# Kernel optimization log

Measured on AMD Instinct MI355X. Metric: run time of the kernel, lower is better.

Reference implementation:

```python
import jax, jax.numpy as jnp
import numpy as np

INPUT_DIM = 512
HIDDEN_DIM = 256
REP_DIM = 256
SCORE_HIDDEN = 128


def setup_inputs() -> dict:
    key = jax.random.key(0)
    ks = jax.random.split(key, 12)
    def rn(k, shape, scale=None):
        s = scale if scale is not None else 1.0 / np.sqrt(shape[0])
        return jax.random.normal(k, shape, dtype=jnp.float32) * s
    return {
        "feat_x": jax.random.normal(ks[0], (512, INPUT_DIM), dtype=jnp.float32),
        "feat_pos": jax.random.normal(ks[1], (512, INPUT_DIM), dtype=jnp.float32),
        "feat_neg": jax.random.normal(ks[2], (512, INPUT_DIM), dtype=jnp.float32),
        # g: Linear(input,hidden) -> GELU -> Linear(hidden,rep); stored as x @ W
        "g_w1": rn(ks[3], (INPUT_DIM, HIDDEN_DIM)),
        "g_b1": jnp.zeros((HIDDEN_DIM,), jnp.float32),
        "g_w2": rn(ks[4], (HIDDEN_DIM, REP_DIM)),
        "g_b2": jnp.zeros((REP_DIM,), jnp.float32),
        # out_proj: Linear(rep, input, bias=False)
        "out_w": rn(ks[5], (REP_DIM, INPUT_DIM)),
        # score_net: Linear(3*rep+1, score_hidden) -> GELU -> Linear(score_hidden, 1)
        "s_w1": rn(ks[6], (3 * REP_DIM + 1, SCORE_HIDDEN)),
        "s_b1": jnp.zeros((SCORE_HIDDEN,), jnp.float32),
        "s_w2": rn(ks[7], (SCORE_HIDDEN, 1)),
        "s_b2": jnp.zeros((1,), jnp.float32),
    }


def _gelu(x):
    return jax.nn.gelu(x, approximate=False)  # torch nn.GELU default = exact erf


def _g(x, g_w1, g_b1, g_w2, g_b2):
    return _gelu(x @ g_w1 + g_b1) @ g_w2 + g_b2


def _set_operator(feat_x, feat_set, params):
    g_w1, g_b1, g_w2, g_b2, out_w, s_w1, s_b1, s_w2, s_b2 = params
    x_rep = _g(feat_x, g_w1, g_b1, g_w2, g_b2)   # (n, r)
    y_rep = _g(feat_set, g_w1, g_b1, g_w2, g_b2)  # (m, r)
    n, r = x_rep.shape
    m = y_rep.shape[0]
    x_exp = jnp.broadcast_to(x_rep[:, None, :], (n, m, r))
    y_exp = jnp.broadcast_to(y_rep[None, :, :], (n, m, r))
    delta = y_exp - x_exp                                   # (n, m, r)
    delta_norm = jnp.linalg.norm(delta, axis=-1, keepdims=True)
    score_in = jnp.concatenate([x_exp, y_exp, delta, delta_norm], axis=-1)  # (n, m, 3r+1)
    logits = (_gelu(score_in @ s_w1 + s_b1) @ s_w2 + s_b2)[..., 0]          # (n, m)
    weights = jax.nn.softmax(logits, axis=1)
    set_update_rep = jnp.einsum("nm,nmr->nr", weights, delta)
    return set_update_rep @ out_w


def reference(feat_x, feat_pos, feat_neg, g_w1, g_b1, g_w2, g_b2, out_w, s_w1, s_b1, s_w2, s_b2):
    params = (g_w1, g_b1, g_w2, g_b2, out_w, s_w1, s_b1, s_w2, s_b2)
    s_pos = _set_operator(feat_x, feat_pos, params)
    s_neg = _set_operator(feat_x, feat_neg, params)  # mask_self_neg=False
    return s_pos - s_neg
```

## Files before the change

### kernel.cpp

```cpp
#include <hip/hip_runtime.h>
#include <math.h>

#define NN 512
#define IN 512
#define HD 256
#define RD 256
#define SH 128

__device__ __forceinline__ float gelu_fast(float x){
    const float z  = x * 0.70710678118654752f;
    const float az = fabsf(z);
    const float t  = __builtin_amdgcn_rcpf(fmaf(0.3275911f, az, 1.0f));
    float p = fmaf(1.061405429f, t, -1.453152027f);
    p = fmaf(p, t, 1.421413741f);
    p = fmaf(p, t, -0.284496736f);
    p = fmaf(p, t, 0.254829592f);
    p = p * t;
    const float e = __builtin_amdgcn_exp2f(z * z * -1.4426950408889634f);
    const float E = p * e;
    const float one_plus_erf = (x >= 0.0f) ? (2.0f - E) : E;
    return 0.5f * x * one_plus_erf;
}

__device__ __forceinline__ float gelu2(float u){
    const float az = fabsf(u);
    const float tt = __builtin_amdgcn_rcpf(fmaf(0.23166045f, az, 1.0f));
    float p = fmaf(1.061405429f, tt, -1.453152027f);
    p = fmaf(p, tt, 1.421413741f);
    p = fmaf(p, tt, -0.284496736f);
    p = fmaf(p, tt, 0.254829592f);
    p = p * tt;
    const float e2 = __builtin_amdgcn_exp2f(u * u * -0.72134752044448170f);
    const float Eq = p * e2;
    const float ope = (u >= 0.0f) ? (2.0f - Eq) : Eq;
    return u * ope;
}

__global__ __launch_bounds__(256) void k_rep(
    const float* __restrict__ fx, const float* __restrict__ fp, const float* __restrict__ fn,
    const float* __restrict__ w1, const float* __restrict__ b1,
    const float* __restrict__ w2, const float* __restrict__ b2,
    const float* __restrict__ s_w1,
    float* __restrict__ r_x, float* __restrict__ r_p, float* __restrict__ r_n,
    float* __restrict__ rT_p, float* __restrict__ rT_n,
    float* __restrict__ A_x, float* __restrict__ BT_p, float* __restrict__ BT_n)
{
    __shared__ float xs[4][IN];
    __shared__ float ps[4][4][HD];
    __shared__ float hs[4][HD];
    __shared__ float rloc[4][RD];
    __shared__ float psf[8][4][SH];
    __shared__ float ab4[4][SH];
    const int t = threadIdx.x;
    const int mat = blockIdx.x >> 7;
    const int row0 = (blockIdx.x & 127) << 2;
    const float* src = (mat==0) ? fx : (mat==1) ? fp : fn;

    #pragma unroll
    for (int rep=0; rep<2; rep++){
        const int idx = rep*256 + t;
        const int j = idx >> 7, q = (idx & 127) << 2;
        *(float4*)&xs[j][q] = *(const float4*)&src[(row0+j)*IN + q];
    }
    __syncthreads();

    const int cg = t & 63, s = t >> 6;
    const int c0 = cg << 2;

    {
        float4 acc[4];
        #pragma unroll
        for (int j=0;j<4;j++) acc[j] = make_float4(0.f,0.f,0.f,0.f);
        const float* wp = w1 + (s*128)*HD + c0;
        #pragma unroll 8
        for (int ii=0; ii<128; ii++){
            float4 w = *(const float4*)wp; wp += HD;
            const int i = s*128 + ii;
            #pragma unroll
            for (int j=0;j<4;j++){
                const float xv = xs[j][i];
                acc[j].x = fmaf(xv, w.x, acc[j].x);
                acc[j].y = fmaf(xv, w.y, acc[j].y);
                acc[j].z = fmaf(xv, w.z, acc[j].z);
                acc[j].w = fmaf(xv, w.w, acc[j].w);
            }
        }
        #pragma unroll
        for (int j=0;j<4;j++) *(float4*)&ps[s][j][c0] = acc[j];
    }
    __syncthreads();

    #pragma unroll
    for (int rep=0; rep<4; rep++){
        const int idx = rep*256 + t;
        const int j = idx >> 8, c = idx & 255;
        const float v = b1[c] + ps[0][j][c] + ps[1][j][c] + ps[2][j][c] + ps[3][j][c];
        hs[j][c] = gelu_fast(v);
    }
    __syncthreads();

    {
        float4 acc[4];
        #pragma unroll
        for (int j=0;j<4;j++) acc[j] = make_float4(0.f,0.f,0.f,0.f);
        const float* wp = w2 + (s*64)*RD + c0;
        #pragma unroll 8
        for (int ii=0; ii<64; ii++){
            float4 w = *(const float4*)wp; wp += RD;
            const int i = s*64 + ii;
            #pragma unroll
            for (int j=0;j<4;j++){
                const float xv = hs[j][i];
                acc[j].x = fmaf(xv, w.x, acc[j].x);
                acc[j].y = fmaf(xv, w.y, acc[j].y);
                acc[j].z = fmaf(xv, w.z, acc[j].z);
                acc[j].w = fmaf(xv, w.w, acc[j].w);
            }
        }
        #pragma unroll
        for (int j=0;j<4;j++) *(float4*)&ps[s][j][c0] = acc[j];
    }
    __syncthreads();

    float* rout = (mat==0) ? r_x : (mat==1) ? r_p : r_n;
    #pragma unroll
    for (int rep=0; rep<4; rep++){
        const int idx = rep*256 + t;
        const int j = idx >> 8, c = idx & 255;
        const float v = b2[c] + ps[0][j][c] + ps[1][j][c] + ps[2][j][c] + ps[3][j][c];
        rloc[j][c] = v;
        rout[(row0+j)*RD + c] = v;
    }
    __syncthreads();

    if (mat){
        float* rT = (mat==1) ? rT_p : rT_n;
        float4 q = make_float4(rloc[0][t], rloc[1][t], rloc[2][t], rloc[3][t]);
        *(float4*)&rT[t*NN + row0] = q;
    }

    {
        const int cg2 = t & 31, s2 = t >> 5;
        const int cc0 = cg2 << 2;
        const float sgn = (mat==0) ? -1.0f : 1.0f;
        const int base1 = (mat==0) ? 0 : 256;
        const float* p1 = s_w1 + (base1 + s2*32)*SH + cc0;
        const float* p3 = s_w1 + (512   + s2*32)*SH + cc0;
        float4 a[4];
        #pragma unroll
        for (int j=0;j<4;j++) a[j] = make_float4(0.f,0.f,0.f,0.f);
        #pragma unroll 8
        for (int ii=0; ii<32; ii++){
            float4 wa = *(const float4*)p1; p1 += SH;
            float4 wd = *(const float4*)p3; p3 += SH;
            float4 w;
            w.x = fmaf(sgn, wd.x, wa.x);
            w.y = fmaf(sgn, wd.y, wa.y);
            w.z = fmaf(sgn, wd.z, wa.z);
            w.w = fmaf(sgn, wd.w, wa.w);
            const int i = s2*32 + ii;
            #pragma unroll
            for (int j=0;j<4;j++){
                const float xv = rloc[j][i];
                a[j].x = fmaf(xv, w.x, a[j].x);
                a[j].y = fmaf(xv, w.y, a[j].y);
                a[j].z = fmaf(xv, w.z, a[j].z);
                a[j].w = fmaf(xv, w.w, a[j].w);
            }
        }
        #pragma unroll
        for (int j=0;j<4;j++) *(float4*)&psf[s2][j][cc0] = a[j];
    }
    __syncthreads();

    #pragma unroll
    for (int rep=0; rep<2; rep++){
        const int idx = rep*256 + t;
        const int j = idx >> 7, c = idx & 127;
        float v = 0.f;
        #pragma unroll
        for (int ss=0; ss<8; ss++) v += psf[ss][j][c];
        if (mat==0) A_x[(row0+j)*SH + c] = v;
        else        ab4[j][c] = v;
    }
    __syncthreads();
    if (mat && t < 128){
        float* BT = (mat==1) ? BT_p : BT_n;
        float4 q = make_float4(ab4[0][t], ab4[1][t], ab4[2][t], ab4[3][t]);
        *(float4*)&BT[t*NN + row0] = q;
    }
}

__global__ __launch_bounds__(256) void k_sd(
    const float* __restrict__ r_x, const float* __restrict__ rT_p, const float* __restrict__ rT_n,
    const float* __restrict__ A_x, const float* __restrict__ BT_p, const float* __restrict__ BT_n,
    const float* __restrict__ s_w1, const float* __restrict__ s_b1,
    const float* __restrict__ s_w2,
    float* __restrict__ E_p, float* __restrict__ E_n, float* __restrict__ Spart)
{
    __shared__ float2 xs2[RD];
    __shared__ float4 cmb[SH];
    __shared__ float pda[2][128];
    __shared__ float pdb[2][128];
    __shared__ float pdc[2][128];
    __shared__ float nx[2];
    __shared__ float ssum[2][2];
    const int t = threadIdx.x;
    const int set = blockIdx.x >> 10;
    const int rem = blockIdx.x & 1023;
    const int n0 = (rem >> 2) << 1;
    const int mt = rem & 3;
    const int mbase = mt << 7;
    const int tm = t & 127, kh = t >> 7;
    const int m = mbase + tm;
    const float* yT = set ? rT_n : rT_p;
    const float* BT = set ? BT_n : BT_p;
    float* E = set ? E_n : E_p;

    xs2[t] = make_float2(r_x[n0*RD + t], r_x[(n0+1)*RD + t]);
    if (t < SH){
        const float b1v = s_b1[t];
        cmb[t] = make_float4(A_x[n0*SH + t] + b1v,
                             A_x[(n0+1)*SH + t] + b1v,
                             s_w1[768*SH + t],
                             0.5f * s_w2[t]);
    }
    __syncthreads();

    if (t < 128){
        const int w = t >> 6, l = t & 63;
        float v = 0.f;
        #pragma unroll
        for (int q=0;q<4;q++){
            const float2 e = xs2[l + 64*q];
            const float ev = w ? e.y : e.x;
            v = fmaf(ev, ev, v);
        }
        #pragma unroll
        for (int off=32; off>=1; off>>=1) v += __shfl_xor(v, off);
        if (l==0) nx[w] = v;
    }

    float d0=0.f, d1=0.f, ny=0.f;
    {
        const float* yp = yT + (kh << 7)*NN + m;
        #pragma unroll 16
        for (int rr=0; rr<128; rr++){
            const float y = yp[rr*NN];
            const float2 xv = xs2[(kh << 7) + rr];
            d0 = fmaf(xv.x, y, d0);
            d1 = fmaf(xv.y, y, d1);
            ny = fmaf(y, y, ny);
        }
    }
    pda[kh][tm] = d0; pdb[kh][tm] = d1; pdc[kh][tm] = ny;
    __syncthreads();
    d0 += pda[1-kh][tm]; d1 += pdb[1-kh][tm]; ny += pdc[1-kh][tm];
    const float dn0 = sqrtf(fmaxf(fmaf(-2.f, d0, nx[0] + ny), 0.f));
    const float dn1 = sqrtf(fmaxf(fmaf(-2.f, d1, nx[1] + ny), 0.f));

    float acc0 = 0.f, acc1 = 0.f;
    {
        const float* bp = BT + (kh << 6)*NN + m;
        #pragma unroll 4
        for (int kk=0; kk<64; kk++){
            const float b = bp[kk*NN];
            const float4 c = cmb[(kh << 6) + kk];
            const float u0 = fmaf(dn0, c.z, c.x + b);
            const float u1 = fmaf(dn1, c.z, c.y + b);
            acc0 = fmaf(c.w, gelu2(u0), acc0);
            acc1 = fmaf(c.w, gelu2(u1), acc1);
        }
    }
    __syncthreads();
    pda[kh][tm] = acc0; pdb[kh][tm] = acc1;
    __syncthreads();
    if (kh == 0){
        const float ev0 = __builtin_amdgcn_exp2f((acc0 + pda[1][tm]) * 1.4426950408889634f);
        const float ev1 = __builtin_amdgcn_exp2f((acc1 + pdb[1][tm]) * 1.4426950408889634f);
        E[n0*NN + m]     = ev0;
        E[(n0+1)*NN + m] = ev1;
        float v0 = ev0, v1 = ev1;
        #pragma unroll
        for (int off=32; off>=1; off>>=1){ v0 += __shfl_xor(v0, off); v1 += __shfl_xor(v1, off); }
        if ((t & 63) == 0){
            ssum[tm >> 6][0] = v0;
            ssum[tm >> 6][1] = v1;
        }
    }
    __syncthreads();
    if (t < 2)
        Spart[(set*4 + mt)*NN + n0 + t] = ssum[0][t] + ssum[1][t];
}

__global__ __launch_bounds__(1024) void k_fin(
    const float* __restrict__ E_p, const float* __restrict__ E_n,
    const float* __restrict__ Spart,
    const float* __restrict__ r_p, const float* __restrict__ r_n,
    const float* __restrict__ out_w, float* __restrict__ out)
{
    __shared__ float wgt[2][2][NN];
    __shared__ float psA[16][2][RD];
    __shared__ float dv[2][RD];
    __shared__ float sinv[4];
    const int t = threadIdx.x;
    const int n0 = blockIdx.x << 1;

    if (t < 4){
        const int se = t >> 1, j = t & 1;
        float S = 0.f;
        #pragma unroll
        for (int q=0;q<4;q++) S += Spart[(se*4+q)*NN + n0 + j];
        sinv[t] = 1.0f / S;
    }
    __syncthreads();
    #pragma unroll
    for (int rep=0; rep<2; rep++){
        const int idx = (rep << 10) + t;
        const int j = (idx >> 9) & 1, m = idx & 511;
        const float* E = rep ? E_n : E_p;
        wgt[rep][j][m] = E[(n0+j)*NN + m] * sinv[rep*2 + j];
    }
    __syncthreads();

    {
        const int cg = t & 63, sl = t >> 6;
        const int c0 = cg << 2;
        const int se = sl >> 3;
        const int m0 = (sl & 7) << 6;
        const float* rsrc = se ? r_n : r_p;
        float4 a0 = make_float4(0.f,0.f,0.f,0.f), a1 = a0;
        const float* rp = rsrc + m0*RD + c0;
        #pragma unroll 8
        for (int mm=0; mm<64; mm++){
            const float4 rv = *(const float4*)rp; rp += RD;
            const float w0 = wgt[se][0][m0+mm];
            const float w1v = wgt[se][1][m0+mm];
            a0.x = fmaf(w0, rv.x, a0.x); a0.y = fmaf(w0, rv.y, a0.y);
            a0.z = fmaf(w0, rv.z, a0.z); a0.w = fmaf(w0, rv.w, a0.w);
            a1.x = fmaf(w1v, rv.x, a1.x); a1.y = fmaf(w1v, rv.y, a1.y);
            a1.z = fmaf(w1v, rv.z, a1.z); a1.w = fmaf(w1v, rv.w, a1.w);
        }
        *(float4*)&psA[sl][0][c0] = a0;
        *(float4*)&psA[sl][1][c0] = a1;
    }
    __syncthreads();
    if (t < 512){
        const int j = t >> 8, c = t & 255;
        float v = 0.f;
        #pragma unroll
        for (int ss=0; ss<8; ss++)  v += psA[ss][j][c];
        #pragma unroll
        for (int ss=8; ss<16; ss++) v -= psA[ss][j][c];
        dv[j][c] = v;
    }
    __syncthreads();

    {
        const int col = t & 511, j = t >> 9;
        float o = 0.f;
        const float* wo = out_w + col;
        #pragma unroll 8
        for (int r=0; r<RD; r++){ o = fmaf(dv[j][r], *wo, o); wo += IN; }
        out[(n0+j)*IN + col] = o;
    }
}

extern "C" void kernel_launch(void* const* d_in, const int* in_sizes, int n_in,
                              void* d_out, int out_size, void* d_ws, size_t ws_size,
                              hipStream_t stream)
{
    const float* fx  = (const float*)d_in[0];
    const float* fp  = (const float*)d_in[1];
    const float* fn  = (const float*)d_in[2];
    const float* gw1 = (const float*)d_in[3];
    const float* gb1 = (const float*)d_in[4];
    const float* gw2 = (const float*)d_in[5];
    const float* gb2 = (const float*)d_in[6];
    const float* ow  = (const float*)d_in[7];
    const float* sw1 = (const float*)d_in[8];
    const float* sb1 = (const float*)d_in[9];
    const float* sw2 = (const float*)d_in[10];
    float* out = (float*)d_out;

    float* ws   = (float*)d_ws;
    float* r_x  = ws;
    float* r_p  = r_x  + 131072;
    float* r_n  = r_p  + 131072;
    float* rT_p = r_n  + 131072;
    float* rT_n = rT_p + 131072;
    float* A_x  = rT_n + 131072;
    float* BT_p = A_x  + 65536;
    float* BT_n = BT_p + 65536;
    float* E_p  = BT_n + 65536;
    float* E_n  = E_p  + 262144;
    float* Spar = E_n  + 262144;

    hipLaunchKernelGGL(k_rep, dim3(384), dim3(256), 0, stream,
                       fx, fp, fn, gw1, gb1, gw2, gb2, sw1,
                       r_x, r_p, r_n, rT_p, rT_n, A_x, BT_p, BT_n);
    hipLaunchKernelGGL(k_sd, dim3(2048), dim3(256), 0, stream,
                       r_x, rT_p, rT_n, A_x, BT_p, BT_n,
                       sw1, sb1, sw2, E_p, E_n, Spar);
    hipLaunchKernelGGL(k_fin, dim3(256), dim3(1024), 0, stream,
                       E_p, E_n, Spar, r_p, r_n, ow, out);
}
```

Before: 160.0 us.

## Retile rep kernel to 8 rows per block and split final stage into two kernels

The representation kernel now processes 8 rows per block with a 2-way k-split, reads inputs straight from global instead of staging them, and keeps transposed hidden/rep tiles in shared memory so each step does vector LDS reads. This halves the number of weight passes per row. The final weighted-sum/out-projection kernel is split into k_dv, which builds partial sums over 8 m-slices across 1024 blocks, and k_out, which reduces those partials and does the out_w projection across 1024 blocks. The goal is more parallelism and better weight reuse, at the cost of an extra launch and an extra partial-sum buffer written to and read back from global memory.

```diff
diff --git a/kernel.cpp b/kernel.cpp
--- a/kernel.cpp
+++ b/kernel.cpp
@@ -36,7 +36,7 @@
     return u * ope;
 }
 
-__global__ __launch_bounds__(256) void k_rep(
+__global__ __launch_bounds__(256) void k_rep8(
     const float* __restrict__ fx, const float* __restrict__ fp, const float* __restrict__ fn,
     const float* __restrict__ w1, const float* __restrict__ b1,
     const float* __restrict__ w2, const float* __restrict__ b2,
@@ -45,149 +45,127 @@
     float* __restrict__ rT_p, float* __restrict__ rT_n,
     float* __restrict__ A_x, float* __restrict__ BT_p, float* __restrict__ BT_n)
 {
-    __shared__ float xs[4][IN];
-    __shared__ float ps[4][4][HD];
-    __shared__ float hs[4][HD];
-    __shared__ float rloc[4][RD];
-    __shared__ float psf[8][4][SH];
-    __shared__ float ab4[4][SH];
+    __shared__ float ps[2][8][256];
+    __shared__ float hsT[256][8];
+    __shared__ float rlocT[256][8];
     const int t = threadIdx.x;
-    const int mat = blockIdx.x >> 7;
-    const int row0 = (blockIdx.x & 127) << 2;
+    const int mat = blockIdx.x >> 6;
+    const int row0 = (blockIdx.x & 63) << 3;
     const float* src = (mat==0) ? fx : (mat==1) ? fp : fn;
 
+    const int cg = t & 127, ks = t >> 7;
+    const int c0 = cg << 1;
+
+    {
+        float2 a[8];
+        #pragma unroll
+        for (int j=0;j<8;j++) a[j] = make_float2(0.f,0.f);
+        const float* wp = w1 + (ks << 8)*HD + c0;
+        const float* xb = src + row0*IN + (ks << 8);
+        #pragma unroll 8
+        for (int ii=0; ii<256; ii++){
+            const float2 w = *(const float2*)wp; wp += HD;
+            #pragma unroll
+            for (int j=0;j<8;j++){
+                const float xv = xb[j*IN + ii];
+                a[j].x = fmaf(xv, w.x, a[j].x);
+                a[j].y = fmaf(xv, w.y, a[j].y);
+            }
+        }
+        #pragma unroll
+        for (int j=0;j<8;j++) *(float2*)&ps[ks][j][c0] = a[j];
+    }
+    __syncthreads();
+
     #pragma unroll
-    for (int rep=0; rep<2; rep++){
+    for (int rep=0; rep<8; rep++){
         const int idx = rep*256 + t;
-        const int j = idx >> 7, q = (idx & 127) << 2;
-        *(float4*)&xs[j][q] = *(const float4*)&src[(row0+j)*IN + q];
-    }
-    __syncthreads();
-
-    const int cg = t & 63, s = t >> 6;
-    const int c0 = cg << 2;
-
-    {
-        float4 acc[4];
-        #pragma unroll
-        for (int j=0;j<4;j++) acc[j] = make_float4(0.f,0.f,0.f,0.f);
-        const float* wp = w1 + (s*128)*HD + c0;
+        const int j = idx >> 8, c = idx & 255;
+        const float v = b1[c] + ps[0][j][c] + ps[1][j][c];
+        hsT[c][j] = gelu_fast(v);
+    }
+    __syncthreads();
+
+    {
+        float2 a[8];
+        #pragma unroll
+        for (int j=0;j<8;j++) a[j] = make_float2(0.f,0.f);
+        const float* wp = w2 + (ks << 7)*RD + c0;
         #pragma unroll 8
         for (int ii=0; ii<128; ii++){
-            float4 w = *(const float4*)wp; wp += HD;
-            const int i = s*128 + ii;
-            #pragma unroll
-            for (int j=0;j<4;j++){
-                const float xv = xs[j][i];
-                acc[j].x = fmaf(xv, w.x, acc[j].x);
-                acc[j].y = fmaf(xv, w.y, acc[j].y);
-                acc[j].z = fmaf(xv, w.z, acc[j].z);
-                acc[j].w = fmaf(xv, w.w, acc[j].w);
-            }
-        }
-        #pragma unroll
-        for (int j=0;j<4;j++) *(float4*)&ps[s][j][c0] = acc[j];
+            const float2 w = *(const float2*)wp; wp += RD;
+            const int i = (ks << 7) + ii;
+            const float4 h0 = *(const float4*)&hsT[i][0];
+            const float4 h1 = *(const float4*)&hsT[i][4];
+            a[0].x = fmaf(h0.x, w.x, a[0].x); a[0].y = fmaf(h0.x, w.y, a[0].y);
+            a[1].x = fmaf(h0.y, w.x, a[1].x); a[1].y = fmaf(h0.y, w.y, a[1].y);
+            a[2].x = fmaf(h0.z, w.x, a[2].x); a[2].y = fmaf(h0.z, w.y, a[2].y);
+            a[3].x = fmaf(h0.w, w.x, a[3].x); a[3].y = fmaf(h0.w, w.y, a[3].y);
+            a[4].x = fmaf(h1.x, w.x, a[4].x); a[4].y = fmaf(h1.x, w.y, a[4].y);
+            a[5].x = fmaf(h1.y, w.x, a[5].x); a[5].y = fmaf(h1.y, w.y, a[5].y);
+            a[6].x = fmaf(h1.z, w.x, a[6].x); a[6].y = fmaf(h1.z, w.y, a[6].y);
+            a[7].x = fmaf(h1.w, w.x, a[7].x); a[7].y = fmaf(h1.w, w.y, a[7].y);
+        }
+        #pragma unroll
+        for (int j=0;j<8;j++) *(float2*)&ps[ks][j][c0] = a[j];
+    }
+    __syncthreads();
+
+    {
+        float* rout = (mat==0) ? r_x : (mat==1) ? r_p : r_n;
+        float* rT   = (mat==1) ? rT_p : rT_n;
+        #pragma unroll
+        for (int rep=0; rep<8; rep++){
+            const int idx = rep*256 + t;
+            const int j = idx >> 8, c = idx & 255;
+            const float v = b2[c] + ps[0][j][c] + ps[1][j][c];
+            rout[(row0+j)*RD + c] = v;
+            rlocT[c][j] = v;
+            if (mat) rT[c*NN + row0 + j] = v;
+        }
+    }
+    __syncthreads();
+
+    float* psf = &ps[0][0][0];
+    {
+        const int cg2 = t & 63, ks2 = t >> 6;
+        const int cc0 = cg2 << 1;
+        const float sgn = (mat==0) ? -1.0f : 1.0f;
+        const int base1 = (mat==0) ? 0 : 256;
+        const float* p1 = s_w1 + (base1 + (ks2 << 6))*SH + cc0;
+        const float* p3 = s_w1 + (512   + (ks2 << 6))*SH + cc0;
+        float2 a[8];
+        #pragma unroll
+        for (int j=0;j<8;j++) a[j] = make_float2(0.f,0.f);
+        #pragma unroll 8
+        for (int ii=0; ii<64; ii++){
+            const float2 wa = *(const float2*)p1; p1 += SH;
+            const float2 wd = *(const float2*)p3; p3 += SH;
+            const float2 w = make_float2(fmaf(sgn, wd.x, wa.x), fmaf(sgn, wd.y, wa.y));
+            const int i = (ks2 << 6) + ii;
+            const float4 r0 = *(const float4*)&rlocT[i][0];
+            const float4 r1 = *(const float4*)&rlocT[i][4];
+            a[0].x = fmaf(r0.x, w.x, a[0].x); a[0].y = fmaf(r0.x, w.y, a[0].y);
+            a[1].x = fmaf(r0.y, w.x, a[1].x); a[1].y = fmaf(r0.y, w.y, a[1].y);
+            a[2].x = fmaf(r0.z, w.x, a[2].x); a[2].y = fmaf(r0.z, w.y, a[2].y);
+            a[3].x = fmaf(r0.w, w.x, a[3].x); a[3].y = fmaf(r0.w, w.y, a[3].y);
+            a[4].x = fmaf(r1.x, w.x, a[4].x); a[4].y = fmaf(r1.x, w.y, a[4].y);
+            a[5].x = fmaf(r1.y, w.x, a[5].x); a[5].y = fmaf(r1.y, w.y, a[5].y);
+            a[6].x = fmaf(r1.z, w.x, a[6].x); a[6].y = fmaf(r1.z, w.y, a[6].y);
+            a[7].x = fmaf(r1.w, w.x, a[7].x); a[7].y = fmaf(r1.w, w.y, a[7].y);
+        }
+        #pragma unroll
+        for (int j=0;j<8;j++) *(float2*)&psf[((ks2 << 3) + j)*SH + cc0] = a[j];
     }
     __syncthreads();
 
     #pragma unroll
     for (int rep=0; rep<4; rep++){
         const int idx = rep*256 + t;
-        const int j = idx >> 8, c = idx & 255;
-        const float v = b1[c] + ps[0][j][c] + ps[1][j][c] + ps[2][j][c] + ps[3][j][c];
-        hs[j][c] = gelu_fast(v);
-    }
-    __syncthreads();
-
-    {
-        float4 acc[4];
-        #pragma unroll
-        for (int j=0;j<4;j++) acc[j] = make_float4(0.f,0.f,0.f,0.f);
-        const float* wp = w2 + (s*64)*RD + c0;
-        #pragma unroll 8
-        for (int ii=0; ii<64; ii++){
-            float4 w = *(const float4*)wp; wp += RD;
-            const int i = s*64 + ii;
-            #pragma unroll
-            for (int j=0;j<4;j++){
-                const float xv = hs[j][i];
-                acc[j].x = fmaf(xv, w.x, acc[j].x);
-                acc[j].y = fmaf(xv, w.y, acc[j].y);
-                acc[j].z = fmaf(xv, w.z, acc[j].z);
-                acc[j].w = fmaf(xv, w.w, acc[j].w);
-            }
-        }
-        #pragma unroll
-        for (int j=0;j<4;j++) *(float4*)&ps[s][j][c0] = acc[j];
-    }
-    __syncthreads();
-
-    float* rout = (mat==0) ? r_x : (mat==1) ? r_p : r_n;
-    #pragma unroll
-    for (int rep=0; rep<4; rep++){
-        const int idx = rep*256 + t;
-        const int j = idx >> 8, c = idx & 255;
-        const float v = b2[c] + ps[0][j][c] + ps[1][j][c] + ps[2][j][c] + ps[3][j][c];
-        rloc[j][c] = v;
-        rout[(row0+j)*RD + c] = v;
-    }
-    __syncthreads();
-
-    if (mat){
-        float* rT = (mat==1) ? rT_p : rT_n;
-        float4 q = make_float4(rloc[0][t], rloc[1][t], rloc[2][t], rloc[3][t]);
-        *(float4*)&rT[t*NN + row0] = q;
-    }
-
-    {
-        const int cg2 = t & 31, s2 = t >> 5;
-        const int cc0 = cg2 << 2;
-        const float sgn = (mat==0) ? -1.0f : 1.0f;
-        const int base1 = (mat==0) ? 0 : 256;
-        const float* p1 = s_w1 + (base1 + s2*32)*SH + cc0;
-        const float* p3 = s_w1 + (512   + s2*32)*SH + cc0;
-        float4 a[4];
-        #pragma unroll
-        for (int j=0;j<4;j++) a[j] = make_float4(0.f,0.f,0.f,0.f);
-        #pragma unroll 8
-        for (int ii=0; ii<32; ii++){
-            float4 wa = *(const float4*)p1; p1 += SH;
-            float4 wd = *(const float4*)p3; p3 += SH;
-            float4 w;
-            w.x = fmaf(sgn, wd.x, wa.x);
-            w.y = fmaf(sgn, wd.y, wa.y);
-            w.z = fmaf(sgn, wd.z, wa.z);
-            w.w = fmaf(sgn, wd.w, wa.w);
-            const int i = s2*32 + ii;
-            #pragma unroll
-            for (int j=0;j<4;j++){
-                const float xv = rloc[j][i];
-                a[j].x = fmaf(xv, w.x, a[j].x);
-                a[j].y = fmaf(xv, w.y, a[j].y);
-                a[j].z = fmaf(xv, w.z, a[j].z);
-                a[j].w = fmaf(xv, w.w, a[j].w);
-            }
-        }
-        #pragma unroll
-        for (int j=0;j<4;j++) *(float4*)&psf[s2][j][cc0] = a[j];
-    }
-    __syncthreads();
-
-    #pragma unroll
-    for (int rep=0; rep<2; rep++){
-        const int idx = rep*256 + t;
         const int j = idx >> 7, c = idx & 127;
-        float v = 0.f;
-        #pragma unroll
-        for (int ss=0; ss<8; ss++) v += psf[ss][j][c];
+        const float v = psf[j*SH+c] + psf[(8+j)*SH+c] + psf[(16+j)*SH+c] + psf[(24+j)*SH+c];
         if (mat==0) A_x[(row0+j)*SH + c] = v;
-        else        ab4[j][c] = v;
-    }
-    __syncthreads();
-    if (mat && t < 128){
-        float* BT = (mat==1) ? BT_p : BT_n;
-        float4 q = make_float4(ab4[0][t], ab4[1][t], ab4[2][t], ab4[3][t]);
-        *(float4*)&BT[t*NN + row0] = q;
+        else        ((mat==1) ? BT_p : BT_n)[c*NN + row0 + j] = v;
     }
 }
 
@@ -293,76 +271,97 @@
         Spart[(set*4 + mt)*NN + n0 + t] = ssum[0][t] + ssum[1][t];
 }
 
-__global__ __launch_bounds__(1024) void k_fin(
+__global__ __launch_bounds__(256) void k_dv(
     const float* __restrict__ E_p, const float* __restrict__ E_n,
     const float* __restrict__ Spart,
     const float* __restrict__ r_p, const float* __restrict__ r_n,
-    const float* __restrict__ out_w, float* __restrict__ out)
+    float* __restrict__ psum)
 {
-    __shared__ float wgt[2][2][NN];
-    __shared__ float psA[16][2][RD];
-    __shared__ float dv[2][RD];
-    __shared__ float sinv[4];
+    __shared__ float rinv[8];
+    __shared__ float wbuf[2][64][4];
     const int t = threadIdx.x;
-    const int n0 = blockIdx.x << 1;
-
-    if (t < 4){
-        const int se = t >> 1, j = t & 1;
+    const int nt = blockIdx.x >> 3;
+    const int ms = blockIdx.x & 7;
+    const int n0 = nt << 2, mbase = ms << 6;
+
+    if (t < 8){
+        const int se = t >> 2, n = n0 + (t & 3);
         float S = 0.f;
         #pragma unroll
-        for (int q=0;q<4;q++) S += Spart[(se*4+q)*NN + n0 + j];
-        sinv[t] = 1.0f / S;
+        for (int q=0;q<4;q++) S += Spart[(se*4+q)*NN + n];
+        rinv[t] = 1.0f / S;
     }
     __syncthreads();
     #pragma unroll
     for (int rep=0; rep<2; rep++){
-        const int idx = (rep << 10) + t;
-        const int j = (idx >> 9) & 1, m = idx & 511;
-        const float* E = rep ? E_n : E_p;
-        wgt[rep][j][m] = E[(n0+j)*NN + m] * sinv[rep*2 + j];
-    }
-    __syncthreads();
-
-    {
-        const int cg = t & 63, sl = t >> 6;
-        const int c0 = cg << 2;
-        const int se = sl >> 3;
-        const int m0 = (sl & 7) << 6;
-        const float* rsrc = se ? r_n : r_p;
-        float4 a0 = make_float4(0.f,0.f,0.f,0.f), a1 = a0;
-        const float* rp = rsrc + m0*RD + c0;
-        #pragma unroll 8
+        const int idx = rep*256 + t;
+        const int se = idx >> 8, j = (idx >> 6) & 3, mm = idx & 63;
+        const float* E = se ? E_n : E_p;
+        wbuf[se][mm][j] = E[(n0+j)*NN + mbase + mm] * rinv[se*4 + j];
+    }
+    __syncthreads();
+
+    float acc[4] = {0.f,0.f,0.f,0.f};
+    {
+        const float* rp = r_p + mbase*RD + t;
+        #pragma unroll 4
         for (int mm=0; mm<64; mm++){
-            const float4 rv = *(const float4*)rp; rp += RD;
-            const float w0 = wgt[se][0][m0+mm];
-            const float w1v = wgt[se][1][m0+mm];
-            a0.x = fmaf(w0, rv.x, a0.x); a0.y = fmaf(w0, rv.y, a0.y);
-            a0.z = fmaf(w0, rv.z, a0.z); a0.w = fmaf(w0, rv.w, a0.w);
-            a1.x = fmaf(w1v, rv.x, a1.x); a1.y = fmaf(w1v, rv.y, a1.y);
-            a1.z = fmaf(w1v, rv.z, a1.z); a1.w = fmaf(w1v, rv.w, a1.w);
-        }
-        *(float4*)&psA[sl][0][c0] = a0;
-        *(float4*)&psA[sl][1][c0] = a1;
-    }
-    __syncthreads();
-    if (t < 512){
-        const int j = t >> 8, c = t & 255;
+            const float rv = *rp; rp += RD;
+            const float4 wa = *(const float4*)&wbuf[0][mm][0];
+            acc[0]=fmaf(wa.x,rv,acc[0]); acc[1]=fmaf(wa.y,rv,acc[1]);
+            acc[2]=fmaf(wa.z,rv,acc[2]); acc[3]=fmaf(wa.w,rv,acc[3]);
+        }
+    }
+    {
+        const float* rn = r_n + mbase*RD + t;
+        #pragma unroll 4
+        for (int mm=0; mm<64; mm++){
+            const float rv = -(*rn); rn += RD;
+            const float4 wa = *(const float4*)&wbuf[1][mm][0];
+            acc[0]=fmaf(wa.x,rv,acc[0]); acc[1]=fmaf(wa.y,rv,acc[1]);
+            acc[2]=fmaf(wa.z,rv,acc[2]); acc[3]=fmaf(wa.w,rv,acc[3]);
+        }
+    }
+    float* P = psum + ms*(NN*RD);
+    #pragma unroll
+    for (int j=0;j<4;j++) P[(n0+j)*RD + t] = acc[j];
+}
+
+__global__ __launch_bounds__(256) void k_out(
+    const float* __restrict__ psum, const float* __restrict__ out_w,
+    float* __restrict__ out)
+{
+    __shared__ float dv2[2][RD];
+    __shared__ float ps[2][2][128];
+    const int t = threadIdx.x;
+    const int nt = blockIdx.x >> 2;
+    const int cb = (blockIdx.x & 3) << 7;
+    const int n0 = nt << 1;
+
+    #pragma unroll
+    for (int j=0;j<2;j++){
         float v = 0.f;
         #pragma unroll
-        for (int ss=0; ss<8; ss++)  v += psA[ss][j][c];
-        #pragma unroll
-        for (int ss=8; ss<16; ss++) v -= psA[ss][j][c];
-        dv[j][c] = v;
-    }
-    __syncthreads();
-
-    {
-        const int col = t & 511, j = t >> 9;
-        float o = 0.f;
-        const float* wo = out_w + col;
-        #pragma unroll 8
-        for (int r=0; r<RD; r++){ o = fmaf(dv[j][r], *wo, o); wo += IN; }
-        out[(n0+j)*IN + col] = o;
+        for (int ms=0; ms<8; ms++) v += psum[ms*(NN*RD) + (n0+j)*RD + t];
+        dv2[j][t] = v;
+    }
+    __syncthreads();
+
+    const int cc = t & 127, s = t >> 7;
+    float a0 = 0.f, a1 = 0.f;
+    const float* wo = out_w + (s*128)*IN + cb + cc;
+    #pragma unroll 4
+    for (int rr=0; rr<128; rr++){
+        const float w = *wo; wo += IN;
+        a0 = fmaf(dv2[0][s*128 + rr], w, a0);
+        a1 = fmaf(dv2[1][s*128 + rr], w, a1);
+    }
+    ps[s][0][cc] = a0;
+    ps[s][1][cc] = a1;
+    __syncthreads();
+    {
+        const int j = t >> 7, c = t & 127;
+        out[(n0+j)*IN + cb + c] = ps[0][j][c] + ps[1][j][c];
     }
 }
 
@@ -395,13 +394,16 @@
     float* E_p  = BT_n + 65536;
     float* E_n  = E_p  + 262144;
     float* Spar = E_n  + 262144;
-
-    hipLaunchKernelGGL(k_rep, dim3(384), dim3(256), 0, stream,
+    float* psum = Spar + 4096;
+
+    hipLaunchKernelGGL(k_rep8, dim3(192), dim3(256), 0, stream,
                        fx, fp, fn, gw1, gb1, gw2, gb2, sw1,
                        r_x, r_p, r_n, rT_p, rT_n, A_x, BT_p, BT_n);
     hipLaunchKernelGGL(k_sd, dim3(2048), dim3(256), 0, stream,
                        r_x, rT_p, rT_n, A_x, BT_p, BT_n,
                        sw1, sb1, sw2, E_p, E_n, Spar);
-    hipLaunchKernelGGL(k_fin, dim3(256), dim3(1024), 0, stream,
-                       E_p, E_n, Spar, r_p, r_n, ow, out);
-}
+    hipLaunchKernelGGL(k_dv, dim3(1024), dim3(256), 0, stream,
+                       E_p, E_n, Spar, r_p, r_n, psum);
+    hipLaunchKernelGGL(k_out, dim3(1024), dim3(256), 0, stream,
+                       psum, ow, out);
+}
```

After: 191.4 us. 19.6% more time.

## Fuse weighted delta aggregation into score kernel and widen rep kernel blocks

Applied to the files above, without the earlier changes.

The score kernel no longer writes the unnormalized exp weights E to global memory. Each block now multiplies its 128 exp values by the matching y_rep rows and writes per-tile partial sums, which k_fin combines with the softmax denominators and projects through out_w, using more blocks. k_rep moves to 512 threads with a finer reduction split and reuses the ps buffer for the score partials. This removes the E round trip and the heavy k_fin matmul over m, but adds repeated y_rep reads in each k_sd block and a larger partial-sum buffer.

```diff
diff --git a/kernel.cpp b/kernel.cpp
--- a/kernel.cpp
+++ b/kernel.cpp
@@ -36,7 +36,7 @@
     return u * ope;
 }
 
-__global__ __launch_bounds__(256) void k_rep(
+__global__ __launch_bounds__(512) void k_rep(
     const float* __restrict__ fx, const float* __restrict__ fp, const float* __restrict__ fn,
     const float* __restrict__ w1, const float* __restrict__ b1,
     const float* __restrict__ w2, const float* __restrict__ b2,
@@ -46,21 +46,18 @@
     float* __restrict__ A_x, float* __restrict__ BT_p, float* __restrict__ BT_n)
 {
     __shared__ float xs[4][IN];
-    __shared__ float ps[4][4][HD];
+    __shared__ float ps[8][4][HD];
     __shared__ float hs[4][HD];
     __shared__ float rloc[4][RD];
-    __shared__ float psf[8][4][SH];
     __shared__ float ab4[4][SH];
     const int t = threadIdx.x;
     const int mat = blockIdx.x >> 7;
     const int row0 = (blockIdx.x & 127) << 2;
     const float* src = (mat==0) ? fx : (mat==1) ? fp : fn;
 
-    #pragma unroll
-    for (int rep=0; rep<2; rep++){
-        const int idx = rep*256 + t;
-        const int j = idx >> 7, q = (idx & 127) << 2;
-        *(float4*)&xs[j][q] = *(const float4*)&src[(row0+j)*IN + q];
+    {
+        const int j = t >> 7, c4 = (t & 127) << 2;
+        *(float4*)&xs[j][c4] = *(const float4*)&src[(row0+j)*IN + c4];
     }
     __syncthreads();
 
@@ -71,11 +68,11 @@
         float4 acc[4];
         #pragma unroll
         for (int j=0;j<4;j++) acc[j] = make_float4(0.f,0.f,0.f,0.f);
-        const float* wp = w1 + (s*128)*HD + c0;
-        #pragma unroll 8
-        for (int ii=0; ii<128; ii++){
+        const float* wp = w1 + (s*64)*HD + c0;
+        #pragma unroll 8
+        for (int ii=0; ii<64; ii++){
             float4 w = *(const float4*)wp; wp += HD;
-            const int i = s*128 + ii;
+            const int i = s*64 + ii;
             #pragma unroll
             for (int j=0;j<4;j++){
                 const float xv = xs[j][i];
@@ -91,10 +88,12 @@
     __syncthreads();
 
     #pragma unroll
-    for (int rep=0; rep<4; rep++){
-        const int idx = rep*256 + t;
+    for (int rep=0; rep<2; rep++){
+        const int idx = rep*512 + t;
         const int j = idx >> 8, c = idx & 255;
-        const float v = b1[c] + ps[0][j][c] + ps[1][j][c] + ps[2][j][c] + ps[3][j][c];
+        float v = b1[c];
+        #pragma unroll
+        for (int ss=0; ss<8; ss++) v += ps[ss][j][c];
         hs[j][c] = gelu_fast(v);
     }
     __syncthreads();
@@ -103,11 +102,11 @@
         float4 acc[4];
         #pragma unroll
         for (int j=0;j<4;j++) acc[j] = make_float4(0.f,0.f,0.f,0.f);
-        const float* wp = w2 + (s*64)*RD + c0;
-        #pragma unroll 8
-        for (int ii=0; ii<64; ii++){
+        const float* wp = w2 + (s*32)*RD + c0;
+        #pragma unroll 8
+        for (int ii=0; ii<32; ii++){
             float4 w = *(const float4*)wp; wp += RD;
-            const int i = s*64 + ii;
+            const int i = s*32 + ii;
             #pragma unroll
             for (int j=0;j<4;j++){
                 const float xv = hs[j][i];
@@ -124,16 +123,18 @@
 
     float* rout = (mat==0) ? r_x : (mat==1) ? r_p : r_n;
     #pragma unroll
-    for (int rep=0; rep<4; rep++){
-        const int idx = rep*256 + t;
+    for (int rep=0; rep<2; rep++){
+        const int idx = rep*512 + t;
         const int j = idx >> 8, c = idx & 255;
-        const float v = b2[c] + ps[0][j][c] + ps[1][j][c] + ps[2][j][c] + ps[3][j][c];
+        float v = b2[c];
+        #pragma unroll
+        for (int ss=0; ss<8; ss++) v += ps[ss][j][c];
         rloc[j][c] = v;
         rout[(row0+j)*RD + c] = v;
     }
     __syncthreads();
 
-    if (mat){
+    if (mat && t < 256){
         float* rT = (mat==1) ? rT_p : rT_n;
         float4 q = make_float4(rloc[0][t], rloc[1][t], rloc[2][t], rloc[3][t]);
         *(float4*)&rT[t*NN + row0] = q;
@@ -144,13 +145,13 @@
         const int cc0 = cg2 << 2;
         const float sgn = (mat==0) ? -1.0f : 1.0f;
         const int base1 = (mat==0) ? 0 : 256;
-        const float* p1 = s_w1 + (base1 + s2*32)*SH + cc0;
-        const float* p3 = s_w1 + (512   + s2*32)*SH + cc0;
+        const float* p1 = s_w1 + (base1 + s2*16)*SH + cc0;
+        const float* p3 = s_w1 + (512   + s2*16)*SH + cc0;
         float4 a[4];
         #pragma unroll
         for (int j=0;j<4;j++) a[j] = make_float4(0.f,0.f,0.f,0.f);
         #pragma unroll 8
-        for (int ii=0; ii<32; ii++){
+        for (int ii=0; ii<16; ii++){
             float4 wa = *(const float4*)p1; p1 += SH;
             float4 wd = *(const float4*)p3; p3 += SH;
             float4 w;
@@ -158,7 +159,7 @@
             w.y = fmaf(sgn, wd.y, wa.y);
             w.z = fmaf(sgn, wd.z, wa.z);
             w.w = fmaf(sgn, wd.w, wa.w);
-            const int i = s2*32 + ii;
+            const int i = s2*16 + ii;
             #pragma unroll
             for (int j=0;j<4;j++){
                 const float xv = rloc[j][i];
@@ -168,18 +169,18 @@
                 a[j].w = fmaf(xv, w.w, a[j].w);
             }
         }
-        #pragma unroll
-        for (int j=0;j<4;j++) *(float4*)&psf[s2][j][cc0] = a[j];
-    }
-    __syncthreads();
-
-    #pragma unroll
-    for (int rep=0; rep<2; rep++){
-        const int idx = rep*256 + t;
-        const int j = idx >> 7, c = idx & 127;
+        float* psf = &ps[0][0][0];
+        #pragma unroll
+        for (int j=0;j<4;j++) *(float4*)&psf[(s2*4 + j)*SH + cc0] = a[j];
+    }
+    __syncthreads();
+
+    {
+        const float* psf = &ps[0][0][0];
+        const int j = t >> 7, c = t & 127;
         float v = 0.f;
         #pragma unroll
-        for (int ss=0; ss<8; ss++) v += psf[ss][j][c];
+        for (int ss=0; ss<16; ss++) v += psf[(ss*4 + j)*SH + c];
         if (mat==0) A_x[(row0+j)*SH + c] = v;
         else        ab4[j][c] = v;
     }
@@ -194,15 +195,17 @@
 __global__ __launch_bounds__(256) void k_sd(
     const float* __restrict__ r_x, const float* __restrict__ rT_p, const float* __restrict__ rT_n,
     const float* __restrict__ A_x, const float* __restrict__ BT_p, const float* __restrict__ BT_n,
+    const float* __restrict__ r_p, const float* __restrict__ r_n,
     const float* __restrict__ s_w1, const float* __restrict__ s_b1,
     const float* __restrict__ s_w2,
-    float* __restrict__ E_p, float* __restrict__ E_n, float* __restrict__ Spart)
+    float* __restrict__ psum, float* __restrict__ Spart)
 {
     __shared__ float2 xs2[RD];
     __shared__ float4 cmb[SH];
     __shared__ float pda[2][128];
     __shared__ float pdb[2][128];
     __shared__ float pdc[2][128];
+    __shared__ float2 evb[128];
     __shared__ float nx[2];
     __shared__ float ssum[2][2];
     const int t = threadIdx.x;
@@ -215,7 +218,6 @@
     const int m = mbase + tm;
     const float* yT = set ? rT_n : rT_p;
     const float* BT = set ? BT_n : BT_p;
-    float* E = set ? E_n : E_p;
 
     xs2[t] = make_float2(r_x[n0*RD + t], r_x[(n0+1)*RD + t]);
     if (t < SH){
@@ -278,8 +280,7 @@
     if (kh == 0){
         const float ev0 = __builtin_amdgcn_exp2f((acc0 + pda[1][tm]) * 1.4426950408889634f);
         const float ev1 = __builtin_amdgcn_exp2f((acc1 + pdb[1][tm]) * 1.4426950408889634f);
-        E[n0*NN + m]     = ev0;
-        E[(n0+1)*NN + m] = ev1;
+        evb[tm] = make_float2(ev0, ev1);
         float v0 = ev0, v1 = ev1;
         #pragma unroll
         for (int off=32; off>=1; off>>=1){ v0 += __shfl_xor(v0, off); v1 += __shfl_xor(v1, off); }
@@ -291,73 +292,53 @@
     __syncthreads();
     if (t < 2)
         Spart[(set*4 + mt)*NN + n0 + t] = ssum[0][t] + ssum[1][t];
-}
-
-__global__ __launch_bounds__(1024) void k_fin(
-    const float* __restrict__ E_p, const float* __restrict__ E_n,
-    const float* __restrict__ Spart,
-    const float* __restrict__ r_p, const float* __restrict__ r_n,
+
+    {
+        const float* ry = (set ? r_n : r_p) + mbase*RD + t;
+        float a0 = 0.f, a1 = 0.f;
+        #pragma unroll 8
+        for (int mm=0; mm<128; mm++){
+            const float rv = ry[mm*RD];
+            const float2 w = evb[mm];
+            a0 = fmaf(w.x, rv, a0);
+            a1 = fmaf(w.y, rv, a1);
+        }
+        float* P = psum + ((set*4 + mt)*NN + n0)*RD;
+        P[t]      = a0;
+        P[RD + t] = a1;
+    }
+}
+
+__global__ __launch_bounds__(512) void k_fin(
+    const float* __restrict__ psum, const float* __restrict__ Spart,
     const float* __restrict__ out_w, float* __restrict__ out)
 {
-    __shared__ float wgt[2][2][NN];
-    __shared__ float psA[16][2][RD];
     __shared__ float dv[2][RD];
-    __shared__ float sinv[4];
     const int t = threadIdx.x;
-    const int n0 = blockIdx.x << 1;
-
-    if (t < 4){
-        const int se = t >> 1, j = t & 1;
-        float S = 0.f;
-        #pragma unroll
-        for (int q=0;q<4;q++) S += Spart[(se*4+q)*NN + n0 + j];
-        sinv[t] = 1.0f / S;
-    }
-    __syncthreads();
-    #pragma unroll
-    for (int rep=0; rep<2; rep++){
-        const int idx = (rep << 10) + t;
-        const int j = (idx >> 9) & 1, m = idx & 511;
-        const float* E = rep ? E_n : E_p;
-        wgt[rep][j][m] = E[(n0+j)*NN + m] * sinv[rep*2 + j];
-    }
-    __syncthreads();
-
-    {
-        const int cg = t & 63, sl = t >> 6;
-        const int c0 = cg << 2;
-        const int se = sl >> 3;
-        const int m0 = (sl & 7) << 6;
-        const float* rsrc = se ? r_n : r_p;
-        float4 a0 = make_float4(0.f,0.f,0.f,0.f), a1 = a0;
-        const float* rp = rsrc + m0*RD + c0;
-        #pragma unroll 8
-        for (int mm=0; mm<64; mm++){
-            const float4 rv = *(const float4*)rp; rp += RD;
-            const float w0 = wgt[se][0][m0+mm];
-            const float w1v = wgt[se][1][m0+mm];
-            a0.x = fmaf(w0, rv.x, a0.x); a0.y = fmaf(w0, rv.y, a0.y);
-            a0.z = fmaf(w0, rv.z, a0.z); a0.w = fmaf(w0, rv.w, a0.w);
-            a1.x = fmaf(w1v, rv.x, a1.x); a1.y = fmaf(w1v, rv.y, a1.y);
-            a1.z = fmaf(w1v, rv.z, a1.z); a1.w = fmaf(w1v, rv.w, a1.w);
-        }
-        *(float4*)&psA[sl][0][c0] = a0;
-        *(float4*)&psA[sl][1][c0] = a1;
-    }
-    __syncthreads();
-    if (t < 512){
+    const int np = blockIdx.x >> 1, ch = blockIdx.x & 1;
+    const int n0 = np << 1;
+
+    {
         const int j = t >> 8, c = t & 255;
-        float v = 0.f;
-        #pragma unroll
-        for (int ss=0; ss<8; ss++)  v += psA[ss][j][c];
-        #pragma unroll
-        for (int ss=8; ss<16; ss++) v -= psA[ss][j][c];
-        dv[j][c] = v;
-    }
-    __syncthreads();
-
-    {
-        const int col = t & 511, j = t >> 9;
+        const int n = n0 + j;
+        float Sp = 0.f, Sn = 0.f;
+        #pragma unroll
+        for (int q=0;q<4;q++){
+            Sp += Spart[q*NN + n];
+            Sn += Spart[(4+q)*NN + n];
+        }
+        float vp = 0.f, vn = 0.f;
+        #pragma unroll
+        for (int q=0;q<4;q++){
+            vp += psum[(q*NN + n)*RD + c];
+            vn += psum[((4+q)*NN + n)*RD + c];
+        }
+        dv[j][c] = vp * (1.0f/Sp) - vn * (1.0f/Sn);
+    }
+    __syncthreads();
+
+    {
+        const int j = t >> 8, col = (ch << 8) + (t & 255);
         float o = 0.f;
         const float* wo = out_w + col;
         #pragma unroll 8
@@ -392,16 +373,15 @@
     float* A_x  = rT_n + 131072;
     float* BT_p = A_x  + 65536;
     float* BT_n = BT_p + 65536;
-    float* E_p  = BT_n + 65536;
-    float* E_n  = E_p  + 262144;
-    float* Spar = E_n  + 262144;
-
-    hipLaunchKernelGGL(k_rep, dim3(384), dim3(256), 0, stream,
+    float* Spar = BT_n + 65536;
+    float* psum = Spar + 4096;
+
+    hipLaunchKernelGGL(k_rep, dim3(384), dim3(512), 0, stream,
                        fx, fp, fn, gw1, gb1, gw2, gb2, sw1,
                        r_x, r_p, r_n, rT_p, rT_n, A_x, BT_p, BT_n);
     hipLaunchKernelGGL(k_sd, dim3(2048), dim3(256), 0, stream,
-                       r_x, rT_p, rT_n, A_x, BT_p, BT_n,
-                       sw1, sb1, sw2, E_p, E_n, Spar);
-    hipLaunchKernelGGL(k_fin, dim3(256), dim3(1024), 0, stream,
-                       E_p, E_n, Spar, r_p, r_n, ow, out);
-}
+                       r_x, rT_p, rT_n, A_x, BT_p, BT_n, r_p, r_n,
+                       sw1, sb1, sw2, psum, Spar);
+    hipLaunchKernelGGL(k_fin, dim3(512), dim3(512), 0, stream,
+                       psum, Spar, ow, out);
+}
```

New measurement: 159.3 us. No clear change (-0.4%).
